# Kernel tuning notes

Measured on AMD Instinct MI355X. Metric: run time of the kernel, lower is better.

## Reference

```python
import jax, jax.numpy as jnp
import numpy as np

N, C, E = 100000, 128, 600000
H = C // 2  # 64


def setup_inputs() -> dict:
    key = jax.random.key(0)
    k1, k2, k3, k4, k5, k6, k7, k8 = jax.random.split(key, 8)
    z_in = jax.random.normal(k1, (N, C), dtype=jnp.float32)
    z_out = jax.random.normal(k2, (N, C), dtype=jnp.float32)
    z_self = jax.random.normal(k3, (N, C), dtype=jnp.float32)
    edge_index = jax.random.randint(k4, (2, E), 0, N, dtype=jnp.int64)
    # MLP params: Linear(C, C//2) -> ELU -> (Dropout eval=no-op) -> Linear(C//2, 1)
    lim1 = 1.0 / np.sqrt(C)
    W1 = jax.random.uniform(k5, (C, H), minval=-lim1, maxval=lim1, dtype=jnp.float32)
    b1 = jax.random.uniform(k6, (H,), minval=-lim1, maxval=lim1, dtype=jnp.float32)
    lim2 = 1.0 / np.sqrt(H)
    W2 = jax.random.uniform(k7, (H, 1), minval=-lim2, maxval=lim2, dtype=jnp.float32)
    b2 = jax.random.uniform(k8, (1,), minval=-lim2, maxval=lim2, dtype=jnp.float32)
    return {"z_in": z_in, "z_out": z_out, "z_self": z_self,
            "edge_index": edge_index, "W1": W1, "b1": b1, "W2": W2, "b2": b2}


def reference(z_in, z_out, z_self, edge_index, W1, b1, W2, b2):
    v1 = z_out + z_self                       # [N, C]
    v2 = z_in + z_self                        # [N, C]
    value = v1[edge_index[0]] * v2[edge_index[1]]  # [E, C] gather + elementwise product
    h = jax.nn.elu(value @ W1 + b1)           # [E, H]; dropout is identity at eval
    logits = h @ W2 + b2                      # [E, 1]
    return jax.nn.sigmoid(logits)
```

## Files before the change

kernel.cpp:

```cpp
#include <hip/hip_runtime.h>
#include <hip/hip_bf16.h>

typedef __attribute__((ext_vector_type(8))) short short8;
typedef __attribute__((ext_vector_type(4))) float f32x4;

__device__ __forceinline__ unsigned short f2bf(float f) {
    unsigned u = __float_as_uint(f);
    u += 0x7fffu + ((u >> 16) & 1u);
    return (unsigned short)(u >> 16);
}
__device__ __forceinline__ float bf2f(unsigned u16) {
    return __uint_as_float(u16 << 16);
}
__device__ __forceinline__ unsigned pk2(float a, float b) {
    return (unsigned)f2bf(a) | ((unsigned)f2bf(b) << 16);
}
__device__ __forceinline__ unsigned mulpack(unsigned a, unsigned b) {
    float alo = bf2f(a & 0xffffu), ahi = bf2f(a >> 16);
    float blo = bf2f(b & 0xffffu), bhi = bf2f(b >> 16);
    return pk2(alo * blo, ahi * bhi);
}

__global__ __launch_bounds__(256) void prep_kernel(
    const float4* __restrict__ zin, const float4* __restrict__ zout,
    const float4* __restrict__ zself,
    ushort4* __restrict__ v1b, ushort4* __restrict__ v2b, int n4)
{
    int i = blockIdx.x * 256 + threadIdx.x;
    if (i >= n4) return;
    float4 o = zout[i], s = zself[i], z = zin[i];
    ushort4 a, b;
    a.x = f2bf(o.x + s.x); a.y = f2bf(o.y + s.y);
    a.z = f2bf(o.z + s.z); a.w = f2bf(o.w + s.w);
    b.x = f2bf(z.x + s.x); b.y = f2bf(z.y + s.y);
    b.z = f2bf(z.z + s.z); b.w = f2bf(z.w + s.w);
    v1b[i] = a; v2b[i] = b;
}

template <bool FUSED>
__global__ __launch_bounds__(256) void edge_kernel(
    const unsigned short* __restrict__ v1b, const unsigned short* __restrict__ v2b,
    const float* __restrict__ zin, const float* __restrict__ zout,
    const float* __restrict__ zself,
    const int* __restrict__ idx,
    const float* __restrict__ W1, const float* __restrict__ b1,
    const float* __restrict__ W2, const float* __restrict__ b2,
    float* __restrict__ out, int E, int ntiles)
{
    __shared__ __align__(16) unsigned short lds_val[4][16][136];

    const int wave = threadIdx.x >> 6;
    const int lane = threadIdx.x & 63;
    const int nn = lane & 15;
    const int q  = lane >> 4;

    short8 Bf[4][4];
#pragma unroll
    for (int kc = 0; kc < 4; kc++)
#pragma unroll
        for (int jt = 0; jt < 4; jt++) {
            short8 v;
#pragma unroll
            for (int t = 0; t < 8; t++)
                v[t] = (short)f2bf(W1[(kc * 32 + q * 8 + t) * 64 + jt * 16 + nn]);
            Bf[kc][jt] = v;
        }
    float bias1[4], w2v[4];
#pragma unroll
    for (int jt = 0; jt < 4; jt++) {
        bias1[jt] = b1[jt * 16 + nn];
        w2v[jt]   = W2[jt * 16 + nn];
    }
    const float b2v = b2[0];

    const int ge   = lane >> 2;
    const int cblk = (lane & 3) * 32;

    const int nwaves = gridDim.x * 4;
    for (int tile = blockIdx.x * 4 + wave; tile < ntiles; tile += nwaves) {
        const int ebase = tile * 16;
        const int ee  = min(ebase + ge, E - 1);
        const int src = idx[ee];
        const int dst = idx[E + ee];

        uint4 prod[4];
        if (FUSED) {
            const uint4* p1 = (const uint4*)(v1b + (size_t)src * 128 + cblk);
            const uint4* p2 = (const uint4*)(v2b + (size_t)dst * 128 + cblk);
#pragma unroll
            for (int i = 0; i < 4; i++) {
                uint4 a = p1[i], c = p2[i];
                prod[i].x = mulpack(a.x, c.x);
                prod[i].y = mulpack(a.y, c.y);
                prod[i].z = mulpack(a.z, c.z);
                prod[i].w = mulpack(a.w, c.w);
            }
        } else {
            const float* po  = zout  + (size_t)src * 128 + cblk;
            const float* ps1 = zself + (size_t)src * 128 + cblk;
            const float* pi  = zin   + (size_t)dst * 128 + cblk;
            const float* ps2 = zself + (size_t)dst * 128 + cblk;
#pragma unroll
            for (int i = 0; i < 4; i++) {
                float4 oa = *(const float4*)(po  + i * 8), ob = *(const float4*)(po  + i * 8 + 4);
                float4 sa = *(const float4*)(ps1 + i * 8), sb = *(const float4*)(ps1 + i * 8 + 4);
                float4 ia = *(const float4*)(pi  + i * 8), ib = *(const float4*)(pi  + i * 8 + 4);
                float4 ta = *(const float4*)(ps2 + i * 8), tb = *(const float4*)(ps2 + i * 8 + 4);
                prod[i].x = pk2((oa.x + sa.x) * (ia.x + ta.x), (oa.y + sa.y) * (ia.y + ta.y));
                prod[i].y = pk2((oa.z + sa.z) * (ia.z + ta.z), (oa.w + sa.w) * (ia.w + ta.w));
                prod[i].z = pk2((ob.x + sb.x) * (ib.x + tb.x), (ob.y + sb.y) * (ib.y + tb.y));
                prod[i].w = pk2((ob.z + sb.z) * (ib.z + tb.z), (ob.w + sb.w) * (ib.w + tb.w));
            }
        }

#pragma unroll
        for (int i = 0; i < 4; i++)
            *(uint4*)&lds_val[wave][ge][cblk + i * 8] = prod[i];

        __builtin_amdgcn_sched_barrier(0);
        __builtin_amdgcn_s_waitcnt(0xC07F);
        __builtin_amdgcn_sched_barrier(0);

        short8 Af[4];
#pragma unroll
        for (int kc = 0; kc < 4; kc++)
            Af[kc] = *(const short8*)&lds_val[wave][nn][kc * 32 + q * 8];

        f32x4 acc[4];
#pragma unroll
        for (int jt = 0; jt < 4; jt++) acc[jt] = (f32x4){0.f, 0.f, 0.f, 0.f};
#pragma unroll
        for (int kc = 0; kc < 4; kc++)
#pragma unroll
            for (int jt = 0; jt < 4; jt++)
                acc[jt] = __builtin_amdgcn_mfma_f32_16x16x32_bf16(
                    Af[kc], Bf[kc][jt], acc[jt], 0, 0, 0);

        float ps[4];
#pragma unroll
        for (int r = 0; r < 4; r++) {
            float s = 0.f;
#pragma unroll
            for (int jt = 0; jt < 4; jt++) {
                float h = acc[jt][r] + bias1[jt];
                h = (h > 0.f) ? h : (__expf(h) - 1.f);
                s += h * w2v[jt];
            }
            ps[r] = s;
        }
#pragma unroll
        for (int off = 1; off < 16; off <<= 1) {
#pragma unroll
            for (int r = 0; r < 4; r++)
                ps[r] += __shfl_xor(ps[r], off, 64);
        }
        if (nn == 0) {
#pragma unroll
            for (int r = 0; r < 4; r++) {
                int e = ebase + q * 4 + r;
                if (e < E) {
                    float x = ps[r] + b2v;
                    out[e] = 1.f / (1.f + __expf(-x));
                }
            }
        }
    }
}

extern "C" void kernel_launch(void* const* d_in, const int* in_sizes, int n_in,
                              void* d_out, int out_size, void* d_ws, size_t ws_size,
                              hipStream_t stream)
{
    const float* zin   = (const float*)d_in[0];
    const float* zout  = (const float*)d_in[1];
    const float* zself = (const float*)d_in[2];
    const int*   idx   = (const int*)d_in[3];
    const float* W1    = (const float*)d_in[4];
    const float* b1    = (const float*)d_in[5];
    const float* W2    = (const float*)d_in[6];
    const float* b2    = (const float*)d_in[7];
    float* out = (float*)d_out;

    const int NC = in_sizes[0];
    const int E  = in_sizes[3] / 2;
    const int ntiles = (E + 15) / 16;
    const size_t need = (size_t)NC * 4;

    if (ws_size >= need) {
        unsigned short* v1b = (unsigned short*)d_ws;
        unsigned short* v2b = v1b + NC;
        const int n4 = NC / 4;
        prep_kernel<<<(n4 + 255) / 256, 256, 0, stream>>>(
            (const float4*)zin, (const float4*)zout, (const float4*)zself,
            (ushort4*)v1b, (ushort4*)v2b, n4);
        edge_kernel<true><<<2048, 256, 0, stream>>>(
            v1b, v2b, zin, zout, zself, idx, W1, b1, W2, b2, out, E, ntiles);
    } else {
        edge_kernel<false><<<2048, 256, 0, stream>>>(
            nullptr, nullptr, zin, zout, zself, idx, W1, b1, W2, b2, out, E, ntiles);
    }
}
```

Measured before the change: 236.1 us.

## Gather edge features directly into MFMA A-fragment layout, drop LDS staging

Each lane now loads the node-feature chunks that match its position in the MFMA A operand (edge = lane&15, k-slice = q), so the product goes straight into registers without a round trip through shared memory and a wait. The bf16 multiply-and-pack also switches from round-to-nearest to truncation through a single byte-permute, which cuts ALU work. In exchange, each lane issues four scattered 16-byte loads per row instead of contiguous 64-byte runs, which may hurt coalescing, and truncation adds a little rounding bias.

Result: slower. 243.5 us (+3.1%).

```diff
diff --git a/kernel.cpp b/kernel.cpp
--- a/kernel.cpp
+++ b/kernel.cpp
@@ -9,16 +9,19 @@
     u += 0x7fffu + ((u >> 16) & 1u);
     return (unsigned short)(u >> 16);
 }
-__device__ __forceinline__ float bf2f(unsigned u16) {
-    return __uint_as_float(u16 << 16);
+
+__device__ __forceinline__ unsigned bfmul_trunc(unsigned a, unsigned b) {
+    float al = __uint_as_float(a << 16);
+    float ah = __uint_as_float(a & 0xffff0000u);
+    float bl = __uint_as_float(b << 16);
+    float bh = __uint_as_float(b & 0xffff0000u);
+    unsigned pl = __float_as_uint(al * bl);
+    unsigned ph = __float_as_uint(ah * bh);
+    return __builtin_amdgcn_perm(ph, pl, 0x07060302u);
 }
-__device__ __forceinline__ unsigned pk2(float a, float b) {
-    return (unsigned)f2bf(a) | ((unsigned)f2bf(b) << 16);
-}
-__device__ __forceinline__ unsigned mulpack(unsigned a, unsigned b) {
-    float alo = bf2f(a & 0xffffu), ahi = bf2f(a >> 16);
-    float blo = bf2f(b & 0xffffu), bhi = bf2f(b >> 16);
-    return pk2(alo * blo, ahi * bhi);
+
+__device__ __forceinline__ unsigned pack_trunc(float lo, float hi) {
+    return __builtin_amdgcn_perm(__float_as_uint(hi), __float_as_uint(lo), 0x07060302u);
 }
 
 __global__ __launch_bounds__(256) void prep_kernel(
@@ -47,8 +50,6 @@
     const float* __restrict__ W2, const float* __restrict__ b2,
     float* __restrict__ out, int E, int ntiles)
 {
-    __shared__ __align__(16) unsigned short lds_val[4][16][136];
-
     const int wave = threadIdx.x >> 6;
     const int lane = threadIdx.x & 63;
     const int nn = lane & 15;
@@ -73,58 +74,51 @@
     }
     const float b2v = b2[0];
 
-    const int ge   = lane >> 2;
-    const int cblk = (lane & 3) * 32;
-
     const int nwaves = gridDim.x * 4;
     for (int tile = blockIdx.x * 4 + wave; tile < ntiles; tile += nwaves) {
         const int ebase = tile * 16;
-        const int ee  = min(ebase + ge, E - 1);
+        const int ee  = min(ebase + nn, E - 1);
         const int src = idx[ee];
         const int dst = idx[E + ee];
 
-        uint4 prod[4];
+        short8 Af[4];
         if (FUSED) {
-            const uint4* p1 = (const uint4*)(v1b + (size_t)src * 128 + cblk);
-            const uint4* p2 = (const uint4*)(v2b + (size_t)dst * 128 + cblk);
+            const uint4* p1 = (const uint4*)(v1b + (size_t)src * 128);
+            const uint4* p2 = (const uint4*)(v2b + (size_t)dst * 128);
+            uint4 a[4], b[4];
 #pragma unroll
-            for (int i = 0; i < 4; i++) {
-                uint4 a = p1[i], c = p2[i];
-                prod[i].x = mulpack(a.x, c.x);
-                prod[i].y = mulpack(a.y, c.y);
-                prod[i].z = mulpack(a.z, c.z);
-                prod[i].w = mulpack(a.w, c.w);
+            for (int kc = 0; kc < 4; kc++) {
+                a[kc] = p1[kc * 4 + q];
+                b[kc] = p2[kc * 4 + q];
+            }
+#pragma unroll
+            for (int kc = 0; kc < 4; kc++) {
+                uint4 p;
+                p.x = bfmul_trunc(a[kc].x, b[kc].x);
+                p.y = bfmul_trunc(a[kc].y, b[kc].y);
+                p.z = bfmul_trunc(a[kc].z, b[kc].z);
+                p.w = bfmul_trunc(a[kc].w, b[kc].w);
+                Af[kc] = __builtin_bit_cast(short8, p);
             }
         } else {
-            const float* po  = zout  + (size_t)src * 128 + cblk;
-            const float* ps1 = zself + (size_t)src * 128 + cblk;
-            const float* pi  = zin   + (size_t)dst * 128 + cblk;
-            const float* ps2 = zself + (size_t)dst * 128 + cblk;
+            const float* po  = zout  + (size_t)src * 128 + q * 8;
+            const float* ps1 = zself + (size_t)src * 128 + q * 8;
+            const float* pi  = zin   + (size_t)dst * 128 + q * 8;
+            const float* ps2 = zself + (size_t)dst * 128 + q * 8;
 #pragma unroll
-            for (int i = 0; i < 4; i++) {
-                float4 oa = *(const float4*)(po  + i * 8), ob = *(const float4*)(po  + i * 8 + 4);
-                float4 sa = *(const float4*)(ps1 + i * 8), sb = *(const float4*)(ps1 + i * 8 + 4);
-                float4 ia = *(const float4*)(pi  + i * 8), ib = *(const float4*)(pi  + i * 8 + 4);
-                float4 ta = *(const float4*)(ps2 + i * 8), tb = *(const float4*)(ps2 + i * 8 + 4);
-                prod[i].x = pk2((oa.x + sa.x) * (ia.x + ta.x), (oa.y + sa.y) * (ia.y + ta.y));
-                prod[i].y = pk2((oa.z + sa.z) * (ia.z + ta.z), (oa.w + sa.w) * (ia.w + ta.w));
-                prod[i].z = pk2((ob.x + sb.x) * (ib.x + tb.x), (ob.y + sb.y) * (ib.y + tb.y));
-                prod[i].w = pk2((ob.z + sb.z) * (ib.z + tb.z), (ob.w + sb.w) * (ib.w + tb.w));
+            for (int kc = 0; kc < 4; kc++) {
+                float4 oa = *(const float4*)(po  + kc * 32), ob = *(const float4*)(po  + kc * 32 + 4);
+                float4 sa = *(const float4*)(ps1 + kc * 32), sb = *(const float4*)(ps1 + kc * 32 + 4);
+                float4 ia = *(const float4*)(pi  + kc * 32), ib = *(const float4*)(pi  + kc * 32 + 4);
+                float4 ta = *(const float4*)(ps2 + kc * 32), tb = *(const float4*)(ps2 + kc * 32 + 4);
+                uint4 p;
+                p.x = pack_trunc((oa.x + sa.x) * (ia.x + ta.x), (oa.y + sa.y) * (ia.y + ta.y));
+                p.y = pack_trunc((oa.z + sa.z) * (ia.z + ta.z), (oa.w + sa.w) * (ia.w + ta.w));
+                p.z = pack_trunc((ob.x + sb.x) * (ib.x + tb.x), (ob.y + sb.y) * (ib.y + tb.y));
+                p.w = pack_trunc((ob.z + sb.z) * (ib.z + tb.z), (ob.w + sb.w) * (ib.w + tb.w));
+                Af[kc] = __builtin_bit_cast(short8, p);
             }
         }
-
-#pragma unroll
-        for (int i = 0; i < 4; i++)
-            *(uint4*)&lds_val[wave][ge][cblk + i * 8] = prod[i];
-
-        __builtin_amdgcn_sched_barrier(0);
-        __builtin_amdgcn_s_waitcnt(0xC07F);
-        __builtin_amdgcn_sched_barrier(0);
-
-        short8 Af[4];
-#pragma unroll
-        for (int kc = 0; kc < 4; kc++)
-            Af[kc] = *(const short8*)&lds_val[wave][nn][kc * 32 + q * 8];
 
         f32x4 acc[4];
 #pragma unroll
```
